# Optimization experiments

Measured on AMD Instinct MI355X. Metric: run time of the kernel, lower is better.

The kernel has to match this reference:

```python
import jax, jax.numpy as jnp
import numpy as np

N = 100000   # nodes
E = 1600000  # edges
D_IN, D_H, D_OUT = 128, 128, 40


def setup_inputs() -> dict:
    key = jax.random.key(0)
    ks = jax.random.split(key, 12)
    feat = jax.random.normal(ks[0], (N, D_IN), dtype=jnp.float32)
    edge_src = jax.random.randint(ks[1], (E,), 0, N, dtype=jnp.int32)
    edge_dst = jax.random.randint(ks[2], (E,), 0, N, dtype=jnp.int32)
    s = 0.05
    W0 = jax.random.normal(ks[3], (D_IN, D_H), dtype=jnp.float32) * s
    W1 = jax.random.normal(ks[4], (D_H, D_H), dtype=jnp.float32) * s
    W2 = jax.random.normal(ks[5], (D_H, D_OUT), dtype=jnp.float32) * s
    b2 = jnp.zeros((D_OUT,), dtype=jnp.float32)
    g0 = jnp.ones((D_H,), dtype=jnp.float32)
    beta0 = jnp.zeros((D_H,), dtype=jnp.float32)
    g1 = jnp.ones((D_H,), dtype=jnp.float32)
    beta1 = jnp.zeros((D_H,), dtype=jnp.float32)
    return dict(feat=feat, edge_src=edge_src, edge_dst=edge_dst,
                W0=W0, W1=W1, W2=W2, b2=b2,
                g0=g0, beta0=beta0, g1=g1, beta1=beta1)


def _degree_norms(edge_src, edge_dst):
    ones = jnp.ones((E,), dtype=jnp.float32)
    out_deg = jax.ops.segment_sum(ones, edge_src, num_segments=N)
    in_deg = jax.ops.segment_sum(ones, edge_dst, num_segments=N)
    # DGL GraphConv norm='both': clamp degree to >=1, pow(-0.5)
    ns = jnp.where(out_deg < 1.0, 1.0, out_deg) ** -0.5  # src norm
    nd = jnp.where(in_deg < 1.0, 1.0, in_deg) ** -0.5    # dst norm
    return ns, nd


def _gcn_conv(h, W, edge_src, edge_dst, ns, nd, bias=None):
    # norm='both': scale src, project (W first since out<=in), aggregate, scale dst
    h = (h * ns[:, None]) @ W                       # [N, out]
    msg = jnp.take(h, edge_src, axis=0)             # [E, out] gather
    agg = jax.ops.segment_sum(msg, edge_dst, num_segments=N)  # scatter-add
    agg = agg * nd[:, None]
    if bias is not None:
        agg = agg + bias
    return agg


def _bn(x, gamma, beta, eps=1e-5):
    mean = jnp.mean(x, axis=0)
    var = jnp.var(x, axis=0)
    return (x - mean) * jax.lax.rsqrt(var + eps) * gamma + beta


def reference(feat, edge_src, edge_dst, W0, W1, W2, b2, g0, beta0, g1, beta1):
    ns, nd = _degree_norms(edge_src, edge_dst)
    # dropout layers are identity in eval mode
    h = _gcn_conv(feat, W0, edge_src, edge_dst, ns, nd)
    h = jax.nn.relu(_bn(h, g0, beta0))
    h = _gcn_conv(h, W1, edge_src, edge_dst, ns, nd)
    h = jax.nn.relu(_bn(h, g1, beta1))
    h = _gcn_conv(h, W2, edge_src, edge_dst, ns, nd, bias=b2)
    return h
```

## Files before the change

kernel.cpp:

```cpp
#include <hip/hip_runtime.h>
#include <hip/hip_bf16.h>


#define D_H 128
#define SCAN_CHUNK 1024

typedef unsigned int uint32;
typedef unsigned short ushort16;
typedef __attribute__((ext_vector_type(8))) short short8v;
typedef __attribute__((ext_vector_type(4))) float float4v;

__device__ __forceinline__ ushort16 f2bf(float f) {
    union { float f; uint32 u; } v;
    v.f = f;
    uint32 u = v.u;
    return (ushort16)((u + 0x7fffu + ((u >> 16) & 1u)) >> 16);
}
__device__ __forceinline__ float2 bf2f2(uint32 u) {
    union { uint32 i; float f; } a, b;
    a.i = u << 16;
    b.i = u & 0xffff0000u;
    return make_float2(a.f, b.f);
}
__device__ __forceinline__ float bf2f(ushort16 h) {
    union { uint32 i; float f; } t;
    t.i = ((uint32)h) << 16;
    return t.f;
}

__global__ __launch_bounds__(256) void bucket_count2_kernel(
    const int* __restrict__ src, const int* __restrict__ dst,
    int* __restrict__ M, int* __restrict__ M2, int E, int nbuck) {
    __shared__ int h[512], h2[512];
    for (int i = threadIdx.x; i < nbuck; i += 256) { h[i] = 0; h2[i] = 0; }
    __syncthreads();
    int j = blockIdx.x;
    int epb = (E + 127) >> 7;
    int estart = j * epb, eend = min(estart + epb, E);
    for (int e = estart + threadIdx.x; e < eend; e += 256) {
        atomicAdd(&h[dst[e] >> 8], 1);
        atomicAdd(&h2[src[e] >> 8], 1);
    }
    __syncthreads();
    for (int b = threadIdx.x; b < nbuck; b += 256) {
        M[(size_t)b * 128 + j] = h[b];
        M2[(size_t)b * 128 + j] = h2[b];
    }
}

__global__ __launch_bounds__(256) void scan1_kernel(const int* __restrict__ deg,
                                                    int* __restrict__ bsum, int n) {
    int tid = threadIdx.x;
    int base = blockIdx.x * SCAN_CHUNK + tid * 4;
    int4 v = make_int4(0, 0, 0, 0);
    if (base + 3 < n) {
        v = *(const int4*)(deg + base);
    } else {
        if (base + 0 < n) v.x = deg[base + 0];
        if (base + 1 < n) v.y = deg[base + 1];
        if (base + 2 < n) v.z = deg[base + 2];
        if (base + 3 < n) v.w = deg[base + 3];
    }
    int s = v.x + v.y + v.z + v.w;
    __shared__ int red[256];
    red[tid] = s;
    __syncthreads();
#pragma unroll
    for (int off = 128; off > 0; off >>= 1) {
        if (tid < off) red[tid] += red[tid + off];
        __syncthreads();
    }
    if (tid == 0) bsum[blockIdx.x] = red[0];
}

__global__ __launch_bounds__(256) void scan3_kernel(const int* __restrict__ deg,
                                                    const int* __restrict__ bsum,
                                                    int* __restrict__ outp,
                                                    int g, int n) {
    int tid = threadIdx.x;
    int base = blockIdx.x * SCAN_CHUNK + tid * 4;
    int4 v = make_int4(0, 0, 0, 0);
    if (base + 3 < n) {
        v = *(const int4*)(deg + base);
    } else {
        if (base + 0 < n) v.x = deg[base + 0];
        if (base + 1 < n) v.y = deg[base + 1];
        if (base + 2 < n) v.z = deg[base + 2];
        if (base + 3 < n) v.w = deg[base + 3];
    }
    int s = v.x + v.y + v.z + v.w;

    __shared__ int bs[128];
    if (tid < 128) bs[tid] = (tid < g) ? bsum[tid] : 0;
    __syncthreads();
#pragma unroll
    for (int off = 1; off < 128; off <<= 1) {
        int t = (tid < 128 && tid >= off) ? bs[tid - off] : 0;
        __syncthreads();
        if (tid < 128) bs[tid] += t;
        __syncthreads();
    }
    int blockbase = (blockIdx.x == 0) ? 0 : bs[blockIdx.x - 1];
    int total = bs[g - 1];

    __shared__ int sc[256];
    sc[tid] = s;
    __syncthreads();
#pragma unroll
    for (int off = 1; off < 256; off <<= 1) {
        int t = (tid >= off) ? sc[tid - off] : 0;
        __syncthreads();
        sc[tid] += t;
        __syncthreads();
    }
    int excl = sc[tid] - s + blockbase;
    int p0 = excl;
    int p1 = p0 + v.x;
    int p2 = p1 + v.y;
    int p3 = p2 + v.z;
    if (base + 3 < n) {
        *(int4*)(outp + base) = make_int4(p0, p1, p2, p3);
    } else {
        if (base + 0 < n) outp[base + 0] = p0;
        if (base + 1 < n) outp[base + 1] = p1;
        if (base + 2 < n) outp[base + 2] = p2;
    }
    if (blockIdx.x == g - 1 && tid == 0) outp[n] = total;
}

__global__ __launch_bounds__(256) void bucket_scatter2_kernel(
    const int* __restrict__ src, const int* __restrict__ dst,
    const int* __restrict__ Mx, const int* __restrict__ Mx2,
    uint32* __restrict__ packed, uint32* __restrict__ sp, int E, int nbuck) {
    __shared__ int cb1[512], c1[512], cb2[512], c2[512];
    int j = blockIdx.x;
    for (int i = threadIdx.x; i < nbuck; i += 256) {
        cb1[i] = Mx[(size_t)i * 128 + j];
        c1[i] = 0;
        cb2[i] = Mx2[(size_t)i * 128 + j];
        c2[i] = 0;
    }
    __syncthreads();
    int epb = (E + 127) >> 7;
    int estart = j * epb, eend = min(estart + epb, E);
    for (int e = estart + threadIdx.x; e < eend; e += 256) {
        int s = src[e], d = dst[e];
        int b = d >> 8;
        int r = atomicAdd(&c1[b], 1);
        packed[cb1[b] + r] = ((uint32)s << 8) | (uint32)(d & 255);
        int b2 = s >> 8;
        int r2 = atomicAdd(&c2[b2], 1);
        sp[cb2[b2] + r2] = (uint32)s;
    }
}

__global__ __launch_bounds__(256) void src_count_kernel(
    const uint32* __restrict__ sp, const int* __restrict__ Mx2,
    float* __restrict__ ns, int E, int N, int nbuck) {
    __shared__ int cnt[256];
    int b = blockIdx.x, tid = threadIdx.x;
    int lo = Mx2[(size_t)b * 128];
    int hi = (b == nbuck - 1) ? E : Mx2[(size_t)(b + 1) * 128];
    cnt[tid] = 0;
    __syncthreads();
    for (int e = lo + tid; e < hi; e += 256)
        atomicAdd(&cnt[sp[e] & 255u], 1);
    __syncthreads();
    int node = b * 256 + tid;
    if (node < N) ns[node] = rsqrtf((float)max(cnt[tid], 1));
}

__global__ __launch_bounds__(256) void csr_kernel(
    const uint32* __restrict__ packed, const int* __restrict__ Mx,
    int* __restrict__ row_ptr, float* __restrict__ nd, int* __restrict__ ssrc,
    int E, int N, int nbuck) {
    __shared__ int cnt[256], pos0[256], cur[256], sc[256];
    int b = blockIdx.x, tid = threadIdx.x;
    int lo = Mx[(size_t)b * 128];
    int hi = (b == nbuck - 1) ? E : Mx[(size_t)(b + 1) * 128];
    cnt[tid] = 0;
    cur[tid] = 0;
    __syncthreads();
    for (int e = lo + tid; e < hi; e += 256)
        atomicAdd(&cnt[packed[e] & 255u], 1);
    __syncthreads();
    int c = cnt[tid];
    sc[tid] = c;
    __syncthreads();
#pragma unroll
    for (int off = 1; off < 256; off <<= 1) {
        int t = (tid >= off) ? sc[tid - off] : 0;
        __syncthreads();
        sc[tid] += t;
        __syncthreads();
    }
    int excl = sc[tid] - c;
    pos0[tid] = lo + excl;
    int node = b * 256 + tid;
    if (node < N) {
        row_ptr[node] = lo + excl;
        nd[node] = rsqrtf((float)max(c, 1));
    }
    if (b == 0 && tid == 0) row_ptr[N] = E;
    __syncthreads();
    for (int e = lo + tid; e < hi; e += 256) {
        uint32 p = packed[e];
        int local = (int)(p & 255u);
        int r = atomicAdd(&cur[local], 1);
        ssrc[pos0[local] + r] = (int)(p >> 8);
    }
}

__global__ void prepw_kernel(const float* __restrict__ W0, const float* __restrict__ W1,
                             const float* __restrict__ W2,
                             ushort16* __restrict__ Wt0, ushort16* __restrict__ Wt1,
                             ushort16* __restrict__ Wt2) {
    int idx = blockIdx.x * 256 + threadIdx.x;
    if (idx < 16384) {
        int n = idx & 127, k = idx >> 7;
        Wt0[n * 128 + k] = f2bf(W0[k * 128 + n]);
        Wt1[n * 128 + k] = f2bf(W1[k * 128 + n]);
    } else {
        int i2 = idx - 16384;
        int n = i2 >> 7, k = i2 & 127;
        Wt2[n * 128 + k] = (n < 40) ? f2bf(W2[k * 40 + n]) : (ushort16)0;
    }
}

template <bool XBF16, bool FUSE_BN>
__global__ __launch_bounds__(256) void gemm_mfma_kernel(
    const void* __restrict__ Xv, const ushort16* __restrict__ Wt,
    const float* __restrict__ ns, const float* __restrict__ ab,
    ushort16* __restrict__ Yb, int nrows) {
    constexpr int LDK = 72;
    __shared__ short As[128 * LDK];
    __shared__ short Ws[128 * LDK];
    int tid = threadIdx.x;
    int row0 = blockIdx.x * 128;
    int wave = tid >> 6, lane = tid & 63;
    int wm = (wave >> 1) * 64, wn = (wave & 1) * 64;
    int l15 = lane & 15, quad = lane >> 4;
    float4v acc[4][4] = {{}};

#pragma unroll
    for (int p = 0; p < 2; ++p) {
        int k0 = p * 64;
        {
            int srow = tid >> 1;
            int half = (tid & 1) * 32;
            int grow = row0 + srow;
            bool ok = grow < nrows;
            float sc = ok ? ns[grow] : 0.f;
            uint32 outu[16];
            if (XBF16) {
                const uint4* xp = (const uint4*)((const uint32*)Xv +
                                                 (size_t)grow * 64 + ((k0 + half) >> 1));
                uint4 u4[4];
#pragma unroll
                for (int q = 0; q < 4; ++q)
                    u4[q] = ok ? xp[q] : make_uint4(0, 0, 0, 0);
                const uint32* uu = (const uint32*)u4;
#pragma unroll
                for (int j = 0; j < 16; ++j) {
                    float2 f = bf2f2(uu[j]);
                    if (FUSE_BN) {
                        int c = k0 + half + j * 2;
                        f.x = fmaxf(fmaf(f.x, ab[c], ab[128 + c]), 0.f);
                        f.y = fmaxf(fmaf(f.y, ab[c + 1], ab[128 + c + 1]), 0.f);
                    }
                    outu[j] = (uint32)f2bf(f.x * sc) | ((uint32)f2bf(f.y * sc) << 16);
                }
            } else {
                const float4* xp = (const float4*)((const float*)Xv +
                                                   (size_t)grow * 128 + k0 + half);
                float4 f4[8];
#pragma unroll
                for (int q = 0; q < 8; ++q)
                    f4[q] = ok ? xp[q] : make_float4(0.f, 0.f, 0.f, 0.f);
                const float* ff = (const float*)f4;
#pragma unroll
                for (int j = 0; j < 16; ++j) {
                    float fx = ff[2 * j], fy = ff[2 * j + 1];
                    if (FUSE_BN) {
                        int c = k0 + half + j * 2;
                        fx = fmaxf(fmaf(fx, ab[c], ab[128 + c]), 0.f);
                        fy = fmaxf(fmaf(fy, ab[c + 1], ab[128 + c + 1]), 0.f);
                    }
                    outu[j] = (uint32)f2bf(fx * sc) | ((uint32)f2bf(fy * sc) << 16);
                }
            }
            uint4* dstA = (uint4*)&As[srow * LDK + half];
#pragma unroll
            for (int q = 0; q < 4; ++q) dstA[q] = ((uint4*)outu)[q];
            const uint4* wp = (const uint4*)((const uint32*)Wt +
                                             srow * 64 + ((k0 + half) >> 1));
            uint4* dstW = (uint4*)&Ws[srow * LDK + half];
#pragma unroll
            for (int q = 0; q < 4; ++q) dstW[q] = wp[q];
        }
        __syncthreads();
#pragma unroll
        for (int ks = 0; ks < 2; ++ks) {
            int koff = ks * 32 + quad * 8;
            short8v a[4], b[4];
#pragma unroll
            for (int t = 0; t < 4; ++t)
                a[t] = *(const short8v*)&As[(wm + t * 16 + l15) * LDK + koff];
#pragma unroll
            for (int u = 0; u < 4; ++u)
                b[u] = *(const short8v*)&Ws[(wn + u * 16 + l15) * LDK + koff];
#pragma unroll
            for (int t = 0; t < 4; ++t)
#pragma unroll
                for (int u = 0; u < 4; ++u)
                    acc[t][u] = __builtin_amdgcn_mfma_f32_16x16x32_bf16(
                        a[t], b[u], acc[t][u], 0, 0, 0);
        }
        __syncthreads();
    }
#pragma unroll
    for (int t = 0; t < 4; ++t) {
#pragma unroll
        for (int r = 0; r < 4; ++r) {
            int grow = row0 + wm + t * 16 + quad * 4 + r;
            if (grow < nrows) {
#pragma unroll
                for (int u = 0; u < 4; ++u)
                    Yb[(size_t)grow * 128 + wn + u * 16 + l15] = f2bf(acc[t][u][r]);
            }
        }
    }
}

__global__ __launch_bounds__(256) void gemm_final_mfma_kernel(
    const uint32* __restrict__ Xb, const ushort16* __restrict__ Wt2,
    const float* __restrict__ bias, float* __restrict__ Y, int nrows) {
    constexpr int LDK = 72;
    __shared__ short As[128 * LDK];
    __shared__ short Ws[64 * LDK];
    int tid = threadIdx.x;
    int row0 = blockIdx.x * 128;
    int wave = tid >> 6, lane = tid & 63;
    int wm = (wave >> 1) * 64, wn = (wave & 1) * 32;
    int l15 = lane & 15, quad = lane >> 4;
    float4v acc[4][2] = {{}};

#pragma unroll
    for (int p = 0; p < 2; ++p) {
        int k0 = p * 64;
        {
            int srow = tid >> 1;
            int half = (tid & 1) * 32;
            int grow = row0 + srow;
            bool ok = grow < nrows;
            const uint4* xp = (const uint4*)(Xb + (size_t)grow * 64 + ((k0 + half) >> 1));
            uint4 u4[4];
#pragma unroll
            for (int q = 0; q < 4; ++q)
                u4[q] = ok ? xp[q] : make_uint4(0, 0, 0, 0);
            uint4* dstA = (uint4*)&As[srow * LDK + half];
#pragma unroll
            for (int q = 0; q < 4; ++q) dstA[q] = u4[q];
        }
        {
            int srow = tid >> 2;
            int off = (tid & 3) * 16;
            const uint4* wp = (const uint4*)((const uint32*)Wt2 +
                                             srow * 64 + ((k0 + off) >> 1));
            uint4* dw = (uint4*)&Ws[srow * LDK + off];
            dw[0] = wp[0];
            dw[1] = wp[1];
        }
        __syncthreads();
#pragma unroll
        for (int ks = 0; ks < 2; ++ks) {
            int koff = ks * 32 + quad * 8;
            short8v a[4], b[2];
#pragma unroll
            for (int t = 0; t < 4; ++t)
                a[t] = *(const short8v*)&As[(wm + t * 16 + l15) * LDK + koff];
#pragma unroll
            for (int u = 0; u < 2; ++u)
                b[u] = *(const short8v*)&Ws[(wn + u * 16 + l15) * LDK + koff];
#pragma unroll
            for (int t = 0; t < 4; ++t)
#pragma unroll
                for (int u = 0; u < 2; ++u)
                    acc[t][u] = __builtin_amdgcn_mfma_f32_16x16x32_bf16(
                        a[t], b[u], acc[t][u], 0, 0, 0);
        }
        __syncthreads();
    }
#pragma unroll
    for (int t = 0; t < 4; ++t) {
#pragma unroll
        for (int r = 0; r < 4; ++r) {
            int grow = row0 + wm + t * 16 + quad * 4 + r;
            if (grow < nrows) {
#pragma unroll
                for (int u = 0; u < 2; ++u) {
                    int col = wn + u * 16 + l15;
                    if (col < 40)
                        Y[(size_t)grow * 40 + col] = acc[t][u][r] + bias[col];
                }
            }
        }
    }
}

__global__ __launch_bounds__(256) void agg128_kernel(
    const uint32* __restrict__ xwb, const int* __restrict__ row_ptr,
    const int* __restrict__ ssrc, const float* __restrict__ nd,
    uint32* __restrict__ outb, int n) {
    int node = blockIdx.x * 4 + (threadIdx.x >> 6);
    if (node >= n) return;
    int lane = threadIdx.x & 63;
    int beg = row_ptr[node], end = row_ptr[node + 1];
    float x = 0.f, y = 0.f;
    int e = beg;
    int nfull = (end - beg) >> 3;
    if (nfull > 0) {
        int s[8];
        uint32 u[8];
#pragma unroll
        for (int j = 0; j < 8; ++j) s[j] = ssrc[e + j];
#pragma unroll
        for (int j = 0; j < 8; ++j) u[j] = xwb[(size_t)s[j] * 64 + lane];
        e += 8;
        for (int it = 1; it < nfull; ++it, e += 8) {
            int s2[8];
            uint32 u2[8];
#pragma unroll
            for (int j = 0; j < 8; ++j) s2[j] = ssrc[e + j];
#pragma unroll
            for (int j = 0; j < 8; ++j) u2[j] = xwb[(size_t)s2[j] * 64 + lane];
#pragma unroll
            for (int j = 0; j < 8; ++j) {
                float2 v = bf2f2(u[j]);
                x += v.x;
                y += v.y;
            }
#pragma unroll
            for (int j = 0; j < 8; ++j) u[j] = u2[j];
        }
#pragma unroll
        for (int j = 0; j < 8; ++j) {
            float2 v = bf2f2(u[j]);
            x += v.x;
            y += v.y;
        }
    }
    for (; e < end; ++e) {
        float2 v = bf2f2(xwb[(size_t)ssrc[e] * 64 + lane]);
        x += v.x;
        y += v.y;
    }
    float s = nd[node];
    outb[(size_t)node * 64 + lane] =
        (uint32)f2bf(x * s) | ((uint32)f2bf(y * s) << 16);
}

__global__ __launch_bounds__(256) void agg128_bn_kernel(
    const uint32* __restrict__ xwb, const int* __restrict__ row_ptr,
    const int* __restrict__ ssrc, const float* __restrict__ nd,
    const float* __restrict__ ns, const float* __restrict__ ab,
    uint32* __restrict__ outb, int n) {
    int node = blockIdx.x * 4 + (threadIdx.x >> 6);
    if (node >= n) return;
    int lane = threadIdx.x & 63;
    float2 a2 = *(const float2*)&ab[lane * 2];
    float2 b2 = *(const float2*)&ab[128 + lane * 2];
    int beg = row_ptr[node], end = row_ptr[node + 1];
    float x = 0.f, y = 0.f;
    int e = beg;
    int nfull = (end - beg) >> 3;
    if (nfull > 0) {
        int s[8];
        uint32 u[8];
        float sc[8];
#pragma unroll
        for (int j = 0; j < 8; ++j) s[j] = ssrc[e + j];
#pragma unroll
        for (int j = 0; j < 8; ++j) {
            u[j] = xwb[(size_t)s[j] * 64 + lane];
            sc[j] = ns[s[j]];
        }
        e += 8;
        for (int it = 1; it < nfull; ++it, e += 8) {
            int s2[8];
            uint32 u2[8];
            float sc2[8];
#pragma unroll
            for (int j = 0; j < 8; ++j) s2[j] = ssrc[e + j];
#pragma unroll
            for (int j = 0; j < 8; ++j) {
                u2[j] = xwb[(size_t)s2[j] * 64 + lane];
                sc2[j] = ns[s2[j]];
            }
#pragma unroll
            for (int j = 0; j < 8; ++j) {
                float2 v = bf2f2(u[j]);
                x += fmaxf(fmaf(v.x, a2.x, b2.x), 0.f) * sc[j];
                y += fmaxf(fmaf(v.y, a2.y, b2.y), 0.f) * sc[j];
            }
#pragma unroll
            for (int j = 0; j < 8; ++j) { u[j] = u2[j]; sc[j] = sc2[j]; }
        }
#pragma unroll
        for (int j = 0; j < 8; ++j) {
            float2 v = bf2f2(u[j]);
            x += fmaxf(fmaf(v.x, a2.x, b2.x), 0.f) * sc[j];
            y += fmaxf(fmaf(v.y, a2.y, b2.y), 0.f) * sc[j];
        }
    }
    for (; e < end; ++e) {
        int s0 = ssrc[e];
        float2 v0 = bf2f2(xwb[(size_t)s0 * 64 + lane]);
        float sc0 = ns[s0];
        x += fmaxf(fmaf(v0.x, a2.x, b2.x), 0.f) * sc0;
        y += fmaxf(fmaf(v0.y, a2.y, b2.y), 0.f) * sc0;
    }
    float s = nd[node];
    outb[(size_t)node * 64 + lane] =
        (uint32)f2bf(x * s) | ((uint32)f2bf(y * s) << 16);
}


__global__ __launch_bounds__(256) void bn_reduce_kernel(const ushort16* __restrict__ x,
                                                        float* __restrict__ stats, int n) {
    int tid = threadIdx.x;
    int col = tid & 127, half = tid >> 7;
    float s = 0.f, s2 = 0.f;
    for (int r = blockIdx.x * 2 + half; r < n; r += gridDim.x * 2) {
        float v = bf2f(x[(size_t)r * D_H + col]);
        s += v;
        s2 = fmaf(v, v, s2);
    }
    __shared__ float red[256];
    red[tid] = s;
    __syncthreads();
    if (half == 0) atomicAdd(&stats[col], s + red[tid + 128]);
    __syncthreads();
    red[tid] = s2;
    __syncthreads();
    if (half == 0) atomicAdd(&stats[128 + col], s2 + red[tid + 128]);
}

__global__ void bn_finalize_kernel(const float* __restrict__ stats,
                                   const float* __restrict__ g,
                                   const float* __restrict__ beta,
                                   float* __restrict__ ab, float inv_n) {
    int c = threadIdx.x;
    float mean = stats[c] * inv_n;
    float var = stats[128 + c] * inv_n - mean * mean;
    float a = rsqrtf(var + 1e-5f) * g[c];
    ab[c] = a;
    ab[128 + c] = beta[c] - mean * a;
}


extern "C" void kernel_launch(void* const* d_in, const int* in_sizes, int n_in,
                              void* d_out, int out_size, void* d_ws, size_t ws_size,
                              hipStream_t stream) {
    const float* feat = (const float*)d_in[0];
    const int* edge_src = (const int*)d_in[1];
    const int* edge_dst = (const int*)d_in[2];
    const float* W0 = (const float*)d_in[3];
    const float* W1 = (const float*)d_in[4];
    const float* W2 = (const float*)d_in[5];
    const float* b2 = (const float*)d_in[6];
    const float* g0 = (const float*)d_in[7];
    const float* beta0 = (const float*)d_in[8];
    const float* g1 = (const float*)d_in[9];
    const float* beta1 = (const float*)d_in[10];
    float* out = (float*)d_out;

    const int N = in_sizes[0] / D_H;
    const int E = in_sizes[1];
    const int nbuck = (N + 255) >> 8;

    char* p = (char*)d_ws;
    auto alloc = [&](size_t bytes) {
        char* r = p;
        p += (bytes + 255) & ~(size_t)255;
        return r;
    };
    uint32* Ab = (uint32*)alloc((size_t)N * D_H * 2);
    uint32* Bb = (uint32*)alloc((size_t)N * D_H * 2);
    float* ns = (float*)alloc((size_t)N * 4);
    float* nd = (float*)alloc((size_t)N * 4);
    int* row_ptr = (int*)alloc((size_t)(N + 1) * 4);
    int* ssrc = (int*)alloc((size_t)E * 4);
    uint32* packed = (uint32*)alloc((size_t)E * 4);
    uint32* sp = (uint32*)alloc((size_t)E * 4);
    int* M = (int*)alloc((size_t)nbuck * 128 * 4);
    int* Mx = (int*)alloc(((size_t)nbuck * 128 + 4) * 4);
    int* M2 = (int*)alloc((size_t)nbuck * 128 * 4);
    int* Mx2 = (int*)alloc(((size_t)nbuck * 128 + 4) * 4);
    int* bsum = (int*)alloc(256 * 4);
    float* stats0 = (float*)alloc(256 * 4);
    float* stats1 = (float*)alloc(256 * 4);
    float* ab0 = (float*)alloc(256 * 4);
    float* ab1 = (float*)alloc(256 * 4);
    ushort16* Wt0 = (ushort16*)alloc(128 * 128 * 2);
    ushort16* Wt1 = (ushort16*)alloc(128 * 128 * 2);
    ushort16* Wt2 = (ushort16*)alloc(64 * 128 * 2);
    (void)ws_size;

    hipMemsetAsync(stats0, 0, 256 * 4, stream);
    hipMemsetAsync(stats1, 0, 256 * 4, stream);

    const int ggrid = (N + 127) / 128;
    const int agrid = (N + 3) / 4;
    const int nM = nbuck * 128;
    const int sgridM = (nM + SCAN_CHUNK - 1) / SCAN_CHUNK;

    prepw_kernel<<<96, 256, 0, stream>>>(W0, W1, W2, Wt0, Wt1, Wt2);

    bucket_count2_kernel<<<128, 256, 0, stream>>>(edge_src, edge_dst, M, M2, E, nbuck);
    scan1_kernel<<<sgridM, 256, 0, stream>>>(M, bsum, nM);
    scan3_kernel<<<sgridM, 256, 0, stream>>>(M, bsum, Mx, sgridM, nM);
    scan1_kernel<<<sgridM, 256, 0, stream>>>(M2, bsum, nM);
    scan3_kernel<<<sgridM, 256, 0, stream>>>(M2, bsum, Mx2, sgridM, nM);
    bucket_scatter2_kernel<<<128, 256, 0, stream>>>(edge_src, edge_dst, Mx, Mx2,
                                                    packed, sp, E, nbuck);
    csr_kernel<<<nbuck, 256, 0, stream>>>(packed, Mx, row_ptr, nd, ssrc, E, N, nbuck);
    src_count_kernel<<<nbuck, 256, 0, stream>>>(sp, Mx2, ns, E, N, nbuck);

    gemm_mfma_kernel<false, false><<<ggrid, 256, 0, stream>>>(
        feat, Wt0, ns, nullptr, (ushort16*)Bb, N);
    agg128_kernel<<<agrid, 256, 0, stream>>>(Bb, row_ptr, ssrc, nd, Ab, N);
    bn_reduce_kernel<<<512, 256, 0, stream>>>((const ushort16*)Ab, stats0, N);
    bn_finalize_kernel<<<1, 128, 0, stream>>>(stats0, g0, beta0, ab0, 1.0f / N);

    gemm_mfma_kernel<true, true><<<ggrid, 256, 0, stream>>>(
        Ab, Wt1, ns, ab0, (ushort16*)Bb, N);
    agg128_kernel<<<agrid, 256, 0, stream>>>(Bb, row_ptr, ssrc, nd, Ab, N);
    bn_reduce_kernel<<<512, 256, 0, stream>>>((const ushort16*)Ab, stats1, N);
    bn_finalize_kernel<<<1, 128, 0, stream>>>(stats1, g1, beta1, ab1, 1.0f / N);

    agg128_bn_kernel<<<agrid, 256, 0, stream>>>(Ab, row_ptr, ssrc, nd, ns, ab1, Bb, N);
    gemm_final_mfma_kernel<<<ggrid, 256, 0, stream>>>(Bb, Wt2, b2, out, N);
}
```

Baseline: 566.3 us.

## Fuse scan passes, CSR/src-count, BN finalize; vectorize BN reduce; simplify gather loops

```diff
diff --git a/kernel.cpp b/kernel.cpp
--- a/kernel.cpp
+++ b/kernel.cpp
@@ -21,11 +21,6 @@
     a.i = u << 16;
     b.i = u & 0xffff0000u;
     return make_float2(a.f, b.f);
-}
-__device__ __forceinline__ float bf2f(ushort16 h) {
-    union { uint32 i; float f; } t;
-    t.i = ((uint32)h) << 16;
-    return t.f;
 }
 
 __global__ __launch_bounds__(256) void bucket_count2_kernel(
@@ -48,10 +43,14 @@
     }
 }
 
-__global__ __launch_bounds__(256) void scan1_kernel(const int* __restrict__ deg,
-                                                    int* __restrict__ bsum, int n) {
+__global__ __launch_bounds__(256) void scan1f_kernel(
+    const int* __restrict__ M, const int* __restrict__ M2,
+    int* __restrict__ bsum, int g, int n) {
+    int half = (blockIdx.x >= g) ? 1 : 0;
+    int blk = blockIdx.x - half * g;
+    const int* deg = half ? M2 : M;
     int tid = threadIdx.x;
-    int base = blockIdx.x * SCAN_CHUNK + tid * 4;
+    int base = blk * SCAN_CHUNK + tid * 4;
     int4 v = make_int4(0, 0, 0, 0);
     if (base + 3 < n) {
         v = *(const int4*)(deg + base);
@@ -73,12 +72,16 @@
     if (tid == 0) bsum[blockIdx.x] = red[0];
 }
 
-__global__ __launch_bounds__(256) void scan3_kernel(const int* __restrict__ deg,
-                                                    const int* __restrict__ bsum,
-                                                    int* __restrict__ outp,
-                                                    int g, int n) {
+__global__ __launch_bounds__(256) void scan3f_kernel(
+    const int* __restrict__ M, const int* __restrict__ M2,
+    const int* __restrict__ bsum, int* __restrict__ Mx, int* __restrict__ Mx2,
+    int g, int n) {
+    int half = (blockIdx.x >= g) ? 1 : 0;
+    int blk = blockIdx.x - half * g;
+    const int* deg = half ? M2 : M;
+    int* outp = half ? Mx2 : Mx;
     int tid = threadIdx.x;
-    int base = blockIdx.x * SCAN_CHUNK + tid * 4;
+    int base = blk * SCAN_CHUNK + tid * 4;
     int4 v = make_int4(0, 0, 0, 0);
     if (base + 3 < n) {
         v = *(const int4*)(deg + base);
@@ -91,7 +94,7 @@
     int s = v.x + v.y + v.z + v.w;
 
     __shared__ int bs[128];
-    if (tid < 128) bs[tid] = (tid < g) ? bsum[tid] : 0;
+    if (tid < 128) bs[tid] = (tid < g) ? bsum[half * g + tid] : 0;
     __syncthreads();
 #pragma unroll
     for (int off = 1; off < 128; off <<= 1) {
@@ -100,7 +103,7 @@
         if (tid < 128) bs[tid] += t;
         __syncthreads();
     }
-    int blockbase = (blockIdx.x == 0) ? 0 : bs[blockIdx.x - 1];
+    int blockbase = (blk == 0) ? 0 : bs[blk - 1];
     int total = bs[g - 1];
 
     __shared__ int sc[256];
@@ -125,7 +128,7 @@
         if (base + 1 < n) outp[base + 1] = p1;
         if (base + 2 < n) outp[base + 2] = p2;
     }
-    if (blockIdx.x == g - 1 && tid == 0) outp[n] = total;
+    if (blk == g - 1 && tid == 0) outp[n] = total;
 }
 
 __global__ __launch_bounds__(256) void bucket_scatter2_kernel(
@@ -154,35 +157,25 @@
     }
 }
 
-__global__ __launch_bounds__(256) void src_count_kernel(
+__global__ __launch_bounds__(256) void csr_src_kernel(
+    const uint32* __restrict__ packed, const int* __restrict__ Mx,
     const uint32* __restrict__ sp, const int* __restrict__ Mx2,
-    float* __restrict__ ns, int E, int N, int nbuck) {
-    __shared__ int cnt[256];
-    int b = blockIdx.x, tid = threadIdx.x;
-    int lo = Mx2[(size_t)b * 128];
-    int hi = (b == nbuck - 1) ? E : Mx2[(size_t)(b + 1) * 128];
-    cnt[tid] = 0;
-    __syncthreads();
-    for (int e = lo + tid; e < hi; e += 256)
-        atomicAdd(&cnt[sp[e] & 255u], 1);
-    __syncthreads();
-    int node = b * 256 + tid;
-    if (node < N) ns[node] = rsqrtf((float)max(cnt[tid], 1));
-}
-
-__global__ __launch_bounds__(256) void csr_kernel(
-    const uint32* __restrict__ packed, const int* __restrict__ Mx,
-    int* __restrict__ row_ptr, float* __restrict__ nd, int* __restrict__ ssrc,
-    int E, int N, int nbuck) {
-    __shared__ int cnt[256], pos0[256], cur[256], sc[256];
+    int* __restrict__ row_ptr, float* __restrict__ nd, float* __restrict__ ns,
+    int* __restrict__ ssrc, int E, int N, int nbuck) {
+    __shared__ int cnt[256], pos0[256], cur[256], sc[256], cnt2[256];
     int b = blockIdx.x, tid = threadIdx.x;
     int lo = Mx[(size_t)b * 128];
     int hi = (b == nbuck - 1) ? E : Mx[(size_t)(b + 1) * 128];
+    int lo2 = Mx2[(size_t)b * 128];
+    int hi2 = (b == nbuck - 1) ? E : Mx2[(size_t)(b + 1) * 128];
     cnt[tid] = 0;
     cur[tid] = 0;
+    cnt2[tid] = 0;
     __syncthreads();
     for (int e = lo + tid; e < hi; e += 256)
         atomicAdd(&cnt[packed[e] & 255u], 1);
+    for (int e = lo2 + tid; e < hi2; e += 256)
+        atomicAdd(&cnt2[sp[e] & 255u], 1);
     __syncthreads();
     int c = cnt[tid];
     sc[tid] = c;
@@ -200,6 +193,7 @@
     if (node < N) {
         row_ptr[node] = lo + excl;
         nd[node] = rsqrtf((float)max(c, 1));
+        ns[node] = rsqrtf((float)max(cnt2[tid], 1));
     }
     if (b == 0 && tid == 0) row_ptr[N] = E;
     __syncthreads();
@@ -230,17 +224,30 @@
 template <bool XBF16, bool FUSE_BN>
 __global__ __launch_bounds__(256) void gemm_mfma_kernel(
     const void* __restrict__ Xv, const ushort16* __restrict__ Wt,
-    const float* __restrict__ ns, const float* __restrict__ ab,
-    ushort16* __restrict__ Yb, int nrows) {
+    const float* __restrict__ ns, const float* __restrict__ stats,
+    const float* __restrict__ gamma, const float* __restrict__ beta,
+    float invn, ushort16* __restrict__ Yb, int nrows) {
     constexpr int LDK = 72;
     __shared__ short As[128 * LDK];
     __shared__ short Ws[128 * LDK];
+    __shared__ float abl[256];
     int tid = threadIdx.x;
     int row0 = blockIdx.x * 128;
     int wave = tid >> 6, lane = tid & 63;
     int wm = (wave >> 1) * 64, wn = (wave & 1) * 64;
     int l15 = lane & 15, quad = lane >> 4;
     float4v acc[4][4] = {{}};
+
+    if (FUSE_BN) {
+        if (tid < 128) {
+            float mean = stats[tid] * invn;
+            float var = stats[128 + tid] * invn - mean * mean;
+            float a = rsqrtf(var + 1e-5f) * gamma[tid];
+            abl[tid] = a;
+            abl[128 + tid] = beta[tid] - mean * a;
+        }
+        __syncthreads();
+    }
 
 #pragma unroll
     for (int p = 0; p < 2; ++p) {
@@ -265,8 +272,8 @@
                     float2 f = bf2f2(uu[j]);
                     if (FUSE_BN) {
                         int c = k0 + half + j * 2;
-                        f.x = fmaxf(fmaf(f.x, ab[c], ab[128 + c]), 0.f);
-                        f.y = fmaxf(fmaf(f.y, ab[c + 1], ab[128 + c + 1]), 0.f);
+                        f.x = fmaxf(fmaf(f.x, abl[c], abl[128 + c]), 0.f);
+                        f.y = fmaxf(fmaf(f.y, abl[c + 1], abl[128 + c + 1]), 0.f);
                     }
                     outu[j] = (uint32)f2bf(f.x * sc) | ((uint32)f2bf(f.y * sc) << 16);
                 }
@@ -281,11 +288,6 @@
 #pragma unroll
                 for (int j = 0; j < 16; ++j) {
                     float fx = ff[2 * j], fy = ff[2 * j + 1];
-                    if (FUSE_BN) {
-                        int c = k0 + half + j * 2;
-                        fx = fmaxf(fmaf(fx, ab[c], ab[128 + c]), 0.f);
-                        fy = fmaxf(fmaf(fy, ab[c + 1], ab[128 + c + 1]), 0.f);
-                    }
                     outu[j] = (uint32)f2bf(fx * sc) | ((uint32)f2bf(fy * sc) << 16);
                 }
             }
@@ -418,31 +420,13 @@
     int beg = row_ptr[node], end = row_ptr[node + 1];
     float x = 0.f, y = 0.f;
     int e = beg;
-    int nfull = (end - beg) >> 3;
-    if (nfull > 0) {
+    for (; e + 8 <= end; e += 8) {
         int s[8];
+#pragma unroll
+        for (int j = 0; j < 8; ++j) s[j] = ssrc[e + j];
         uint32 u[8];
 #pragma unroll
-        for (int j = 0; j < 8; ++j) s[j] = ssrc[e + j];
-#pragma unroll
         for (int j = 0; j < 8; ++j) u[j] = xwb[(size_t)s[j] * 64 + lane];
-        e += 8;
-        for (int it = 1; it < nfull; ++it, e += 8) {
-            int s2[8];
-            uint32 u2[8];
-#pragma unroll
-            for (int j = 0; j < 8; ++j) s2[j] = ssrc[e + j];
-#pragma unroll
-            for (int j = 0; j < 8; ++j) u2[j] = xwb[(size_t)s2[j] * 64 + lane];
-#pragma unroll
-            for (int j = 0; j < 8; ++j) {
-                float2 v = bf2f2(u[j]);
-                x += v.x;
-                y += v.y;
-            }
-#pragma unroll
-            for (int j = 0; j < 8; ++j) u[j] = u2[j];
-        }
 #pragma unroll
         for (int j = 0; j < 8; ++j) {
             float2 v = bf2f2(u[j]);
@@ -450,10 +434,17 @@
             y += v.y;
         }
     }
-    for (; e < end; ++e) {
-        float2 v = bf2f2(xwb[(size_t)ssrc[e] * 64 + lane]);
-        x += v.x;
-        y += v.y;
+    for (; e + 2 <= end; e += 2) {
+        uint32 u0 = xwb[(size_t)ssrc[e] * 64 + lane];
+        uint32 u1 = xwb[(size_t)ssrc[e + 1] * 64 + lane];
+        float2 v0 = bf2f2(u0), v1 = bf2f2(u1);
+        x += v0.x + v1.x;
+        y += v0.y + v1.y;
+    }
+    if (e < end) {
+        float2 v0 = bf2f2(xwb[(size_t)ssrc[e] * 64 + lane]);
+        x += v0.x;
+        y += v0.y;
     }
     float s = nd[node];
     outb[(size_t)node * 64 + lane] =
@@ -463,48 +454,33 @@
 __global__ __launch_bounds__(256) void agg128_bn_kernel(
     const uint32* __restrict__ xwb, const int* __restrict__ row_ptr,
     const int* __restrict__ ssrc, const float* __restrict__ nd,
-    const float* __restrict__ ns, const float* __restrict__ ab,
-    uint32* __restrict__ outb, int n) {
+    const float* __restrict__ ns, const float* __restrict__ stats,
+    const float* __restrict__ gamma, const float* __restrict__ beta,
+    float invn, uint32* __restrict__ outb, int n) {
     int node = blockIdx.x * 4 + (threadIdx.x >> 6);
     if (node >= n) return;
     int lane = threadIdx.x & 63;
-    float2 a2 = *(const float2*)&ab[lane * 2];
-    float2 b2 = *(const float2*)&ab[128 + lane * 2];
+    int c = lane * 2;
+    float m0 = stats[c] * invn, m1 = stats[c + 1] * invn;
+    float v0_ = stats[128 + c] * invn - m0 * m0;
+    float v1_ = stats[128 + c + 1] * invn - m1 * m1;
+    float a0 = rsqrtf(v0_ + 1e-5f) * gamma[c];
+    float a1 = rsqrtf(v1_ + 1e-5f) * gamma[c + 1];
+    float2 a2 = make_float2(a0, a1);
+    float2 b2 = make_float2(beta[c] - m0 * a0, beta[c + 1] - m1 * a1);
     int beg = row_ptr[node], end = row_ptr[node + 1];
     float x = 0.f, y = 0.f;
     int e = beg;
-    int nfull = (end - beg) >> 3;
-    if (nfull > 0) {
+    for (; e + 8 <= end; e += 8) {
         int s[8];
+#pragma unroll
+        for (int j = 0; j < 8; ++j) s[j] = ssrc[e + j];
         uint32 u[8];
         float sc[8];
-#pragma unroll
-        for (int j = 0; j < 8; ++j) s[j] = ssrc[e + j];
 #pragma unroll
         for (int j = 0; j < 8; ++j) {
             u[j] = xwb[(size_t)s[j] * 64 + lane];
             sc[j] = ns[s[j]];
-        }
-        e += 8;
-        for (int it = 1; it < nfull; ++it, e += 8) {
-            int s2[8];
-            uint32 u2[8];
-            float sc2[8];
-#pragma unroll
-            for (int j = 0; j < 8; ++j) s2[j] = ssrc[e + j];
-#pragma unroll
-            for (int j = 0; j < 8; ++j) {
-                u2[j] = xwb[(size_t)s2[j] * 64 + lane];
-                sc2[j] = ns[s2[j]];
-            }
-#pragma unroll
-            for (int j = 0; j < 8; ++j) {
-                float2 v = bf2f2(u[j]);
-                x += fmaxf(fmaf(v.x, a2.x, b2.x), 0.f) * sc[j];
-                y += fmaxf(fmaf(v.y, a2.y, b2.y), 0.f) * sc[j];
-            }
-#pragma unroll
-            for (int j = 0; j < 8; ++j) { u[j] = u2[j]; sc[j] = sc2[j]; }
         }
 #pragma unroll
         for (int j = 0; j < 8; ++j) {
@@ -525,37 +501,37 @@
         (uint32)f2bf(x * s) | ((uint32)f2bf(y * s) << 16);
 }
 
-
-__global__ __launch_bounds__(256) void bn_reduce_kernel(const ushort16* __restrict__ x,
+__global__ __launch_bounds__(256) void bn_reduce_kernel(const uint4* __restrict__ x4,
                                                         float* __restrict__ stats, int n) {
     int tid = threadIdx.x;
-    int col = tid & 127, half = tid >> 7;
-    float s = 0.f, s2 = 0.f;
-    for (int r = blockIdx.x * 2 + half; r < n; r += gridDim.x * 2) {
-        float v = bf2f(x[(size_t)r * D_H + col]);
-        s += v;
-        s2 = fmaf(v, v, s2);
-    }
-    __shared__ float red[256];
-    red[tid] = s;
-    __syncthreads();
-    if (half == 0) atomicAdd(&stats[col], s + red[tid + 128]);
-    __syncthreads();
-    red[tid] = s2;
-    __syncthreads();
-    if (half == 0) atomicAdd(&stats[128 + col], s2 + red[tid + 128]);
-}
-
-__global__ void bn_finalize_kernel(const float* __restrict__ stats,
-                                   const float* __restrict__ g,
-                                   const float* __restrict__ beta,
-                                   float* __restrict__ ab, float inv_n) {
-    int c = threadIdx.x;
-    float mean = stats[c] * inv_n;
-    float var = stats[128 + c] * inv_n - mean * mean;
-    float a = rsqrtf(var + 1e-5f) * g[c];
-    ab[c] = a;
-    ab[128 + c] = beta[c] - mean * a;
+    int ctile = tid & 15;
+    int rgrp = tid >> 4;
+    float s[8] = {}, s2[8] = {};
+    for (int r = blockIdx.x * 16 + rgrp; r < n; r += gridDim.x * 16) {
+        uint4 u = x4[(size_t)r * 16 + ctile];
+        uint32 uu[4] = {u.x, u.y, u.z, u.w};
+#pragma unroll
+        for (int q = 0; q < 4; ++q) {
+            float2 v = bf2f2(uu[q]);
+            s[q * 2] += v.x;
+            s[q * 2 + 1] += v.y;
+            s2[q * 2] = fmaf(v.x, v.x, s2[q * 2]);
+            s2[q * 2 + 1] = fmaf(v.y, v.y, s2[q * 2 + 1]);
+        }
+    }
+    __shared__ float ls[128], ls2[128];
+    if (tid < 128) { ls[tid] = 0.f; ls2[tid] = 0.f; }
+    __syncthreads();
+#pragma unroll
+    for (int j = 0; j < 8; ++j) {
+        atomicAdd(&ls[ctile * 8 + j], s[j]);
+        atomicAdd(&ls2[ctile * 8 + j], s2[j]);
+    }
+    __syncthreads();
+    if (tid < 128) {
+        atomicAdd(&stats[tid], ls[tid]);
+        atomicAdd(&stats[128 + tid], ls2[tid]);
+    }
 }
 
 
@@ -578,6 +554,7 @@
     const int N = in_sizes[0] / D_H;
     const int E = in_sizes[1];
     const int nbuck = (N + 255) >> 8;
+    const float invN = 1.0f / (float)N;
 
     char* p = (char*)d_ws;
     auto alloc = [&](size_t bytes) {
@@ -600,15 +577,12 @@
     int* bsum = (int*)alloc(256 * 4);
     float* stats0 = (float*)alloc(256 * 4);
     float* stats1 = (float*)alloc(256 * 4);
-    float* ab0 = (float*)alloc(256 * 4);
-    float* ab1 = (float*)alloc(256 * 4);
     ushort16* Wt0 = (ushort16*)alloc(128 * 128 * 2);
     ushort16* Wt1 = (ushort16*)alloc(128 * 128 * 2);
     ushort16* Wt2 = (ushort16*)alloc(64 * 128 * 2);
     (void)ws_size;
 
-    hipMemsetAsync(stats0, 0, 256 * 4, stream);
-    hipMemsetAsync(stats1, 0, 256 * 4, stream);
+    hipMemsetAsync(stats0, 0, 2048, stream);
 
     const int ggrid = (N + 127) / 128;
     const int agrid = (N + 3) / 4;
@@ -618,27 +592,24 @@
     prepw_kernel<<<96, 256, 0, stream>>>(W0, W1, W2, Wt0, Wt1, Wt2);
 
     bucket_count2_kernel<<<128, 256, 0, stream>>>(edge_src, edge_dst, M, M2, E, nbuck);
-    scan1_kernel<<<sgridM, 256, 0, stream>>>(M, bsum, nM);
-    scan3_kernel<<<sgridM, 256, 0, stream>>>(M, bsum, Mx, sgridM, nM);
-    scan1_kernel<<<sgridM, 256, 0, stream>>>(M2, bsum, nM);
-    scan3_kernel<<<sgridM, 256, 0, stream>>>(M2, bsum, Mx2, sgridM, nM);
+    scan1f_kernel<<<2 * sgridM, 256, 0, stream>>>(M, M2, bsum, sgridM, nM);
+    scan3f_kernel<<<2 * sgridM, 256, 0, stream>>>(M, M2, bsum, Mx, Mx2, sgridM, nM);
     bucket_scatter2_kernel<<<128, 256, 0, stream>>>(edge_src, edge_dst, Mx, Mx2,
                                                     packed, sp, E, nbuck);
-    csr_kernel<<<nbuck, 256, 0, stream>>>(packed, Mx, row_ptr, nd, ssrc, E, N, nbuck);
-    src_count_kernel<<<nbuck, 256, 0, stream>>>(sp, Mx2, ns, E, N, nbuck);
+    csr_src_kernel<<<nbuck, 256, 0, stream>>>(packed, Mx, sp, Mx2, row_ptr, nd, ns,
+                                              ssrc, E, N, nbuck);
 
     gemm_mfma_kernel<false, false><<<ggrid, 256, 0, stream>>>(
-        feat, Wt0, ns, nullptr, (ushort16*)Bb, N);
+        feat, Wt0, ns, nullptr, nullptr, nullptr, invN, (ushort16*)Bb, N);
     agg128_kernel<<<agrid, 256, 0, stream>>>(Bb, row_ptr, ssrc, nd, Ab, N);
-    bn_reduce_kernel<<<512, 256, 0, stream>>>((const ushort16*)Ab, stats0, N);
-    bn_finalize_kernel<<<1, 128, 0, stream>>>(stats0, g0, beta0, ab0, 1.0f / N);
+    bn_reduce_kernel<<<512, 256, 0, stream>>>((const uint4*)Ab, stats0, N);
 
     gemm_mfma_kernel<true, true><<<ggrid, 256, 0, stream>>>(
-        Ab, Wt1, ns, ab0, (ushort16*)Bb, N);
+        Ab, Wt1, ns, stats0, g0, beta0, invN, (ushort16*)Bb, N);
     agg128_kernel<<<agrid, 256, 0, stream>>>(Bb, row_ptr, ssrc, nd, Ab, N);
-    bn_reduce_kernel<<<512, 256, 0, stream>>>((const ushort16*)Ab, stats1, N);
-    bn_finalize_kernel<<<1, 128, 0, stream>>>(stats1, g1, beta1, ab1, 1.0f / N);
-
-    agg128_bn_kernel<<<agrid, 256, 0, stream>>>(Ab, row_ptr, ssrc, nd, ns, ab1, Bb, N);
+    bn_reduce_kernel<<<512, 256, 0, stream>>>((const uint4*)Ab, stats1, N);
+
+    agg128_bn_kernel<<<agrid, 256, 0, stream>>>(Ab, row_ptr, ssrc, nd, ns,
+                                                stats1, g1, beta1, invN, Bb, N);
     gemm_final_mfma_kernel<<<ggrid, 256, 0, stream>>>(Bb, Wt2, b2, out, N);
 }
```

After: 495.7 us. 1.14x faster.
